# Optimization experiments

Measured on AMD Instinct MI355X. Metric: run time of the kernel, lower is better.

Reference implementation:

```python
import jax, jax.numpy as jnp
from jax import lax
import numpy as np

POINT_PAIRS = 10000
SIGMA = 0.03
ALPHA = 1.0
MIN_DEPTH = -0.001
MAX_DEPTH = 80.0


def _get_edges(images):
    # images: [n,3,H,W]; Sobel on channel 0, VALID conv then zero-pad by 1 (as in torch code)
    x = images[:, :1]
    kx = jnp.array([[-1., 0., 1.], [-2., 0., 2.], [-1., 0., 1.]], jnp.float32).reshape(1, 1, 3, 3)
    ky = jnp.array([[1., 2., 1.], [0., 0., 0.], [-1., -2., -1.]], jnp.float32).reshape(1, 1, 3, 3)
    gx = lax.conv_general_dilated(x, kx, (1, 1), 'VALID')
    gy = lax.conv_general_dilated(x, ky, (1, 1), 'VALID')
    edges = jnp.sqrt(gx * gx + gy * gy)
    thetas = jnp.arctan2(gy, gx)
    pad = ((0, 0), (0, 0), (1, 1), (1, 1))
    return jnp.pad(edges, pad), jnp.pad(thetas, pad)


def _sample_and_loss(key, inp, tgt, edge, theta, smask):
    # inp/tgt/edge/theta: [H,W] float; smask: [H,W] bool
    H, W = inp.shape
    k1, k2, k3 = jax.random.split(key, 3)
    # edge-guided anchor sampling: uniform over {edge >= 0.1*max} & strict_mask, with replacement
    emask = (edge >= 0.1 * edge.max()) & smask
    p = emask.reshape(-1).astype(jnp.float32)
    p = p / jnp.maximum(p.sum(), 1.0)
    flat_idx = jax.random.choice(k1, H * W, (POINT_PAIRS,), replace=True, p=p)
    sh = flat_idx // W
    sw = flat_idx % W
    th = theta.reshape(-1)[flat_idx]
    # signed step distances along / perpendicular to the edge direction
    dist = jax.random.randint(k2, (4, POINT_PAIRS), 2, 31).astype(jnp.float32)
    sign = jnp.array([-1., -1., 1., 1.], jnp.float32).reshape(4, 1)
    dist = dist * sign
    # random_direct: p<0.5 -> along gradient; else rotate theta by pi/2 (swapped cos/sin)
    pdir = jax.random.uniform(k3) < 0.5
    th2 = ((th + jnp.pi / 2) + jnp.pi) % (2 * jnp.pi) - jnp.pi
    col1 = sw[None, :] + jnp.round(dist * jnp.cos(th)[None, :]).astype(jnp.int32)
    row1 = sh[None, :] + jnp.round(dist * jnp.sin(th)[None, :]).astype(jnp.int32)
    col2 = sw[None, :] + jnp.round(dist * jnp.sin(th2)[None, :]).astype(jnp.int32)
    row2 = sh[None, :] + jnp.round(dist * jnp.cos(th2)[None, :]).astype(jnp.int32)
    col = jnp.where(pdir, col1, col2)  # [4,N]
    row = jnp.where(pdir, row1, row2)
    inb = (col >= 0) & (col <= W - 1) & (row >= 0) & (row <= H - 1)
    valid = jnp.all(inb, axis=0)  # [N]; torch drops these columns, we mask instead
    colc = jnp.clip(col, 0, W - 1)
    rowc = jnp.clip(row, 0, H - 1)
    # pairs (a,b),(b,c),(c,d) -> A = [a,b,c], B = [b,c,d]
    rA = jnp.concatenate([rowc[0], rowc[1], rowc[2]])
    cA = jnp.concatenate([colc[0], colc[1], colc[2]])
    rB = jnp.concatenate([rowc[1], rowc[2], rowc[3]])
    cB = jnp.concatenate([colc[1], colc[2], colc[3]])
    vm = jnp.concatenate([valid, valid, valid]).astype(jnp.float32)  # [3N]
    iA = inp[rA, cA]
    iB = inp[rB, cB]
    tA = tgt[rA, cA]
    tB = tgt[rB, cB]
    # ranking loss
    ratio = (tA + 1e-6) / (tB + 1e-6)
    absdiff = jnp.abs(tA - tB)
    maxdiff = jnp.max(jnp.where(vm > 0, absdiff, 0.0))
    tw = jnp.exp(absdiff / (maxdiff + 1e-6))
    eq = (ratio < 1.0 + SIGMA) & (ratio > 1.0 / (1.0 + SIGMA))
    labels = jnp.where(ratio >= 1.0 + SIGMA, 1.0,
                       jnp.where(ratio <= 1.0 / (1.0 + SIGMA), -1.0, 0.0))
    equal_loss = (iA - iB) ** 2 / tw * eq.astype(jnp.float32)
    unequal_loss = jnp.log1p(jnp.exp((iB - iA) * labels)) * (1.0 - eq.astype(jnp.float32))
    cnt = jnp.maximum(vm.sum(), 1.0)
    loss = ALPHA * jnp.sum(equal_loss * vm) / cnt + jnp.sum(unequal_loss * vm) / cnt
    return loss, vm.sum()


def setup_inputs() -> dict:
    key = jax.random.key(0)
    k1, k2, k3, k4 = jax.random.split(key, 4)
    n, H, W = 8, 1024, 1024
    inputs = jax.random.normal(k1, (n, 1, H, W), jnp.float32)
    targets = jax.random.uniform(k2, (n, 1, H, W), jnp.float32)
    images = jax.random.uniform(k3, (n, 3, H, W), jnp.float32)
    depth_gt = jax.random.uniform(k4, (n, 1, H, W), jnp.float32)
    return {"inputs": inputs, "targets": targets, "images": images, "depth_gt": depth_gt}


def reference(inputs, targets, images, depth_gt):
    n = inputs.shape[0]
    strict = (depth_gt > MIN_DEPTH) & (depth_gt < MAX_DEPTH) & ~(targets == 80.0)
    edges, thetas = _get_edges(images)
    keys = jax.random.split(jax.random.key(42), n)
    losses, counts = jax.vmap(_sample_and_loss)(
        keys, inputs[:, 0], targets[:, 0], edges[:, 0], thetas[:, 0], strict[:, 0])
    return losses.sum() / n, counts.sum() / n
```

## Files before the change

kernel.cpp:

```cpp
#include <hip/hip_runtime.h>
#include <math.h>
#include <stdint.h>

#define NIMG 8
#define HH 1024
#define WW 1024
#define NPIX (HH*WW)
#define PAIRS 10000
#define STRIP 8
#define NSTRIPS 128
#define S1BLOCKS 40
#define WSLOTS (S1BLOCKS*4)
#define FBLK 4
#define QPAIRS (PAIRS/FBLK)

#define OFF_EDGE 0
#define OFF_MD   1024
#define OFF_RES  4096
#define OFF_CTR  4112

__device__ __forceinline__ uint64_t mix64(uint64_t x){
    x += 0x9E3779B97F4A7C15ull;
    x = (x ^ (x >> 30)) * 0xBF58476D1CE4E5B9ull;
    x = (x ^ (x >> 27)) * 0x94D049BB133111EBull;
    return x ^ (x >> 31);
}

__device__ __forceinline__ float block_reduce_max(float v, float* sm){
    for (int off = 32; off; off >>= 1)
        v = fmaxf(v, __shfl_down(v, off));
    int wv = threadIdx.x >> 6, lane = threadIdx.x & 63;
    if (lane == 0) sm[wv] = v;
    __syncthreads();
    if (threadIdx.x == 0)
        sm[0] = fmaxf(fmaxf(sm[0], sm[1]), fmaxf(sm[2], sm[3]));
    __syncthreads();
    float r = sm[0];
    __syncthreads();
    return r;
}

__device__ __forceinline__ float block_reduce_sum(float v, float* sm){
    for (int off = 32; off; off >>= 1)
        v += __shfl_down(v, off);
    int wv = threadIdx.x >> 6, lane = threadIdx.x & 63;
    if (lane == 0) sm[wv] = v;
    __syncthreads();
    if (threadIdx.x == 0)
        sm[0] = sm[0] + sm[1] + sm[2] + sm[3];
    __syncthreads();
    float r = sm[0];
    __syncthreads();
    return r;
}

__device__ __forceinline__ void sobel_at(const float* __restrict__ x, int r, int c,
                                         float& gx, float& gy){
    const float* p0 = x + (size_t)(r-1)*WW + c;
    const float* p1 = x + (size_t)r*WW + c;
    const float* p2 = x + (size_t)(r+1)*WW + c;
    float a = p0[-1], b = p0[0], cc = p0[1];
    float d = p1[-1],             e = p1[1];
    float f = p2[-1], g = p2[0], h = p2[1];
    gx = (cc - a) + 2.0f*(e - d) + (h - f);
    gy = (a + 2.0f*b + cc) - (f + 2.0f*g + h);
}

__device__ __forceinline__ void load16(const float* __restrict__ p, float* d){
    const float4* q = (const float4*)p;
    float4 v0 = q[0], v1 = q[1], v2 = q[2], v3 = q[3];
    d[0]=v0.x; d[1]=v0.y; d[2]=v0.z; d[3]=v0.w;
    d[4]=v1.x; d[5]=v1.y; d[6]=v1.z; d[7]=v1.w;
    d[8]=v2.x; d[9]=v2.y; d[10]=v2.z; d[11]=v2.w;
    d[12]=v3.x; d[13]=v3.y; d[14]=v3.z; d[15]=v3.w;
}

__global__ __launch_bounds__(256) void edgemax_kernel(const float* __restrict__ images,
                                                      float* __restrict__ ws){
    if (blockIdx.x == 0 && threadIdx.x < 17)
        ws[OFF_RES + threadIdx.x] = 0.0f;

    int img  = blockIdx.x & 7;
    int xb   = blockIdx.x >> 3;
    const float* x = images + (size_t)img * 3 * NPIX;
    int wv   = threadIdx.x >> 6;
    int lane = threadIdx.x & 63;
    int strip = xb * 4 + wv;
    int r0 = 1 + strip * STRIP;
    int r1 = min(r0 + STRIP - 1, HH - 2);
    int c0 = lane * 16;

    float a[16], b[16], n[16];
    load16(x + (size_t)(r0-1)*WW + c0, a);
    load16(x + (size_t)r0*WW + c0, b);

    float m = 0.0f;
    for (int r = r0; r <= r1; ++r){
        load16(x + (size_t)(r+1)*WW + c0, n);
        float sx[16], dy[16];
        #pragma unroll
        for (int i = 0; i < 16; ++i){
            sx[i] = a[i] + 2.0f*b[i] + n[i];
            dy[i] = a[i] - n[i];
        }
        float sxl = __shfl_up(sx[15], 1);
        float sxr = __shfl_down(sx[0], 1);
        float dyl = __shfl_up(dy[15], 1);
        float dyr = __shfl_down(dy[0], 1);
        #pragma unroll
        for (int j = 0; j < 16; ++j){
            float sl = (j == 0)  ? sxl : sx[j-1];
            float sr = (j == 15) ? sxr : sx[j+1];
            float dl = (j == 0)  ? dyl : dy[j-1];
            float dr = (j == 15) ? dyr : dy[j+1];
            float gx = sr - sl;
            float gy = dl + 2.0f*dy[j] + dr;
            float e2 = gx*gx + gy*gy;
            int c = c0 + j;
            if (c >= 1 && c <= WW-2) m = fmaxf(m, e2);
        }
        #pragma unroll
        for (int i = 0; i < 16; ++i){ a[i] = b[i]; b[i] = n[i]; }
    }
    for (int off = 32; off; off >>= 1)
        m = fmaxf(m, __shfl_down(m, off));
    if (lane == 0)
        ws[OFF_EDGE + img * NSTRIPS + strip] = m;
}

__global__ __launch_bounds__(256) void sample_kernel(
                               const float* __restrict__ inputs,
                               const float* __restrict__ targets,
                               const float* __restrict__ images,
                               const float* __restrict__ depth_gt,
                               float* __restrict__ ws,
                               float4* __restrict__ recsA,
                               float4* __restrict__ recsB){
    __shared__ float sred[4];
    int img = blockIdx.x & 7;
    int jb  = blockIdx.x >> 3;
    int tid = threadIdx.x;
    int j   = jb * 256 + tid;
    const float* x   = images   + (size_t)img * 3 * NPIX;
    const float* inp = inputs   + (size_t)img * NPIX;
    const float* tgt = targets  + (size_t)img * NPIX;
    const float* dgt = depth_gt + (size_t)img * NPIX;

    float ev = 0.0f;
    if (tid < NSTRIPS) ev = ws[OFF_EDGE + img * NSTRIPS + tid];
    float thr2 = 0.01f * block_reduce_max(ev, sred);

    float mdiff = 0.0f;
    float4 recA = make_float4(0.f, 0.f, 0.f, 0.f);
    float4 recB = make_float4(0.f, 0.f, 0.f, 0.f);

    if (j < PAIRS){
        uint64_t base = ((uint64_t)(img * PAIRS + j)) << 10;
        bool pdir = (mix64(((uint64_t)(NIMG * PAIRS + img)) << 10) & 1ull) != 0ull;

        int sh = -1, sw = -1;
        float gxs = 0.f, gys = 0.f, e2s = 1.f;
        for (int att = 0; att < 900; ++att){
            uint64_t u = mix64(base + (uint64_t)att);
            uint32_t pix = (uint32_t)(u >> 44);
            int r = (int)(pix >> 10);
            int c = (int)(pix & (WW - 1));
            if (r == 0 || r >= HH-1 || c == 0 || c >= WW-1) continue;
            float gx, gy;
            sobel_at(x, r, c, gx, gy);
            float e2 = gx*gx + gy*gy;
            if (!(e2 >= thr2)) continue;
            float dg = dgt[r*WW + c];
            float tg = tgt[r*WW + c];
            if (!(dg > -0.001f && dg < 80.0f && tg != 80.0f)) continue;
            sh = r; sw = c; gxs = gx; gys = gy; e2s = e2;
            break;
        }

        if (sh >= 0){
            float inv = rsqrtf(e2s);
            float cmul = gxs * inv;
            float rmul = gys * inv;
            if (!pdir) cmul = -cmul;

            uint64_t u0 = mix64(base + 1000ull);
            uint64_t u1 = mix64(base + 1001ull);
            float dist[4];
            dist[0] = -(float)(2u + (uint32_t)(u0 & 0xFFFFFFFFull) % 29u);
            dist[1] = -(float)(2u + (uint32_t)(u0 >> 32) % 29u);
            dist[2] =  (float)(2u + (uint32_t)(u1 & 0xFFFFFFFFull) % 29u);
            dist[3] =  (float)(2u + (uint32_t)(u1 >> 32) % 29u);

            int rowc[4], colc[4];
            bool valid = true;
            #pragma unroll
            for (int k = 0; k < 4; ++k){
                int cc2 = sw + (int)rintf(dist[k] * cmul);
                int rr2 = sh + (int)rintf(dist[k] * rmul);
                if (cc2 < 0 || cc2 > WW-1 || rr2 < 0 || rr2 > HH-1) valid = false;
                colc[k] = min(max(cc2, 0), WW-1);
                rowc[k] = min(max(rr2, 0), HH-1);
            }

            if (valid){
                float t4[4], i4[4];
                #pragma unroll
                for (int k = 0; k < 4; ++k){
                    int p = rowc[k]*WW + colc[k];
                    t4[k] = tgt[p];
                    i4[k] = inp[p];
                }
                float d2a[3], ada[3];
                float un = 0.0f;
                #pragma unroll
                for (int k = 0; k < 3; ++k){
                    float tA = t4[k], tB = t4[k+1];
                    float ratio = (tA + 1e-6f) / (tB + 1e-6f);
                    float adk = fabsf(tA - tB);
                    mdiff = fmaxf(mdiff, adk);
                    bool eq = (ratio < 1.03f) && (ratio > 0.9708737864077669f);
                    if (eq){
                        float d = i4[k] - i4[k+1];
                        d2a[k] = d*d; ada[k] = adk;
                    } else {
                        d2a[k] = 0.f; ada[k] = 0.f;
                        float lab = (ratio >= 1.03f) ? 1.0f : -1.0f;
                        un += log1pf(expf((i4[k+1] - i4[k]) * lab));
                    }
                }
                recA = make_float4(d2a[0], d2a[1], d2a[2], un);
                recB = make_float4(ada[0], ada[1], ada[2], 3.0f);
            }
        }
        recsA[img * PAIRS + j] = recA;
        recsB[img * PAIRS + j] = recB;
    }

    for (int off = 32; off; off >>= 1)
        mdiff = fmaxf(mdiff, __shfl_down(mdiff, off));
    if ((tid & 63) == 0)
        ws[OFF_MD + img * WSLOTS + jb*4 + (tid >> 6)] = mdiff;
}

__global__ __launch_bounds__(256) void finish_kernel(
                               float* __restrict__ ws,
                               const float4* __restrict__ recsA,
                               const float4* __restrict__ recsB,
                               float* __restrict__ out){
    __shared__ float sred[4];
    __shared__ unsigned lastflag;
    int img = blockIdx.x & 7;
    int q   = blockIdx.x >> 3;
    int tid = threadIdx.x;

    float mv = 0.0f;
    if (tid < WSLOTS) mv = ws[OFF_MD + img * WSLOTS + tid];
    float md = block_reduce_max(mv, sred);
    float inv = 1.0f / (md + 1e-6f);

    float loss = 0.0f, cnt = 0.0f;
    int base = img * PAIRS + q * QPAIRS;
    for (int r = tid; r < QPAIRS; r += 256){
        float4 A = recsA[base + r];
        float4 B = recsB[base + r];
        loss += A.w
              + A.x * expf(-B.x * inv)
              + A.y * expf(-B.y * inv)
              + A.z * expf(-B.z * inv);
        cnt  += B.w;
    }
    loss = block_reduce_sum(loss, sred);
    cnt  = block_reduce_sum(cnt, sred);

    if (tid == 0){
        atomicAdd(&ws[OFF_RES + img*2 + 0], loss);
        atomicAdd(&ws[OFF_RES + img*2 + 1], cnt);
        __threadfence();
        unsigned old = atomicAdd((unsigned int*)&ws[OFF_CTR], 1u);
        lastflag = (old == (unsigned)(NIMG*FBLK - 1)) ? 1u : 0u;
    }
    __syncthreads();

    if (lastflag){
        __threadfence();
        float val = 0.0f, cv = 0.0f;
        if (tid < NIMG){
            float li = atomicAdd(&ws[OFF_RES + tid*2 + 0], 0.0f);
            float ci = atomicAdd(&ws[OFF_RES + tid*2 + 1], 0.0f);
            val = li / fmaxf(ci, 1.0f);
            cv  = ci;
        }
        for (int off = 4; off; off >>= 1){
            val += __shfl_down(val, off);
            cv  += __shfl_down(cv,  off);
        }
        if (tid == 0){
            out[0] = val / (float)NIMG;
            out[1] = cv  / (float)NIMG;
        }
    }
}

extern "C" void kernel_launch(void* const* d_in, const int* in_sizes, int n_in,
                              void* d_out, int out_size, void* d_ws, size_t ws_size,
                              hipStream_t stream) {
    const float* inputs  = (const float*)d_in[0];
    const float* targets = (const float*)d_in[1];
    const float* images  = (const float*)d_in[2];
    const float* depth   = (const float*)d_in[3];
    float* out = (float*)d_out;

    float* ws     = (float*)d_ws;
    float4* recsA = (float4*)((char*)d_ws + 65536);
    float4* recsB = recsA + (size_t)NIMG * PAIRS;

    hipLaunchKernelGGL(edgemax_kernel, dim3(NSTRIPS/4 * NIMG), dim3(256), 0, stream,
                       images, ws);
    hipLaunchKernelGGL(sample_kernel, dim3(S1BLOCKS * NIMG), dim3(256), 0, stream,
                       inputs, targets, images, depth, ws, recsA, recsB);
    hipLaunchKernelGGL(finish_kernel, dim3(NIMG * FBLK), dim3(256), 0, stream,
                       ws, recsA, recsB, out);
}
```

Before: 38.25 us.

## Fuse finish reduction into sample kernel via last-block-per-image atomics

Merges the separate finish kernel into the sample kernel. Each block publishes its max depth difference with an atomicMax and bumps a per-image counter, and the last block for each image does that image's loss reduction. A second counter picks the final block, which writes the outputs. This removes one kernel launch and its gap, but the per-image tail reduction now runs on one block per image (8 blocks) instead of 32. It also depends on atomic ordering through s_waitcnt instead of a full threadfence.

```diff
diff --git a/kernel.cpp b/kernel.cpp
--- a/kernel.cpp
+++ b/kernel.cpp
@@ -10,14 +10,14 @@
 #define STRIP 8
 #define NSTRIPS 128
 #define S1BLOCKS 40
-#define WSLOTS (S1BLOCKS*4)
-#define FBLK 4
-#define QPAIRS (PAIRS/FBLK)
 
 #define OFF_EDGE 0
-#define OFF_MD   1024
-#define OFF_RES  4096
-#define OFF_CTR  4112
+#define OFF_MDI  4096
+#define OFF_DONE 4104
+#define OFF_GL   4112
+#define OFF_GC   4113
+#define OFF_IMGD 4114
+#define ZERO_N   24
 
 __device__ __forceinline__ uint64_t mix64(uint64_t x){
     x += 0x9E3779B97F4A7C15ull;
@@ -77,8 +77,8 @@
 
 __global__ __launch_bounds__(256) void edgemax_kernel(const float* __restrict__ images,
                                                       float* __restrict__ ws){
-    if (blockIdx.x == 0 && threadIdx.x < 17)
-        ws[OFF_RES + threadIdx.x] = 0.0f;
+    if (blockIdx.x == 0 && threadIdx.x < ZERO_N)
+        ws[OFF_MDI + threadIdx.x] = 0.0f;
 
     int img  = blockIdx.x & 7;
     int xb   = blockIdx.x >> 3;
@@ -128,15 +128,17 @@
         ws[OFF_EDGE + img * NSTRIPS + strip] = m;
 }
 
-__global__ __launch_bounds__(256) void sample_kernel(
+__global__ __launch_bounds__(256) void sample_finish_kernel(
                                const float* __restrict__ inputs,
                                const float* __restrict__ targets,
                                const float* __restrict__ images,
                                const float* __restrict__ depth_gt,
                                float* __restrict__ ws,
                                float4* __restrict__ recsA,
-                               float4* __restrict__ recsB){
+                               float4* __restrict__ recsB,
+                               float* __restrict__ out){
     __shared__ float sred[4];
+    __shared__ unsigned flag1;
     int img = blockIdx.x & 7;
     int jb  = blockIdx.x >> 3;
     int tid = threadIdx.x;
@@ -236,67 +238,45 @@
         recsB[img * PAIRS + j] = recB;
     }
 
-    for (int off = 32; off; off >>= 1)
-        mdiff = fmaxf(mdiff, __shfl_down(mdiff, off));
-    if ((tid & 63) == 0)
-        ws[OFF_MD + img * WSLOTS + jb*4 + (tid >> 6)] = mdiff;
-}
-
-__global__ __launch_bounds__(256) void finish_kernel(
-                               float* __restrict__ ws,
-                               const float4* __restrict__ recsA,
-                               const float4* __restrict__ recsB,
-                               float* __restrict__ out){
-    __shared__ float sred[4];
-    __shared__ unsigned lastflag;
-    int img = blockIdx.x & 7;
-    int q   = blockIdx.x >> 3;
-    int tid = threadIdx.x;
-
-    float mv = 0.0f;
-    if (tid < WSLOTS) mv = ws[OFF_MD + img * WSLOTS + tid];
-    float md = block_reduce_max(mv, sred);
-    float inv = 1.0f / (md + 1e-6f);
-
-    float loss = 0.0f, cnt = 0.0f;
-    int base = img * PAIRS + q * QPAIRS;
-    for (int r = tid; r < QPAIRS; r += 256){
-        float4 A = recsA[base + r];
-        float4 B = recsB[base + r];
-        loss += A.w
-              + A.x * expf(-B.x * inv)
-              + A.y * expf(-B.y * inv)
-              + A.z * expf(-B.z * inv);
-        cnt  += B.w;
+    float mdb = block_reduce_max(mdiff, sred);
+    if (tid == 0){
+        if (mdb > 0.0f)
+            atomicMax((unsigned int*)&ws[OFF_MDI + img], __float_as_uint(mdb));
+        asm volatile("s_waitcnt vmcnt(0)" ::: "memory");
+        unsigned old = atomicAdd((unsigned int*)&ws[OFF_DONE + img], 1u);
+        flag1 = (old == (unsigned)(S1BLOCKS - 1)) ? 1u : 0u;
     }
-    loss = block_reduce_sum(loss, sred);
-    cnt  = block_reduce_sum(cnt, sred);
-
-    if (tid == 0){
-        atomicAdd(&ws[OFF_RES + img*2 + 0], loss);
-        atomicAdd(&ws[OFF_RES + img*2 + 1], cnt);
-        __threadfence();
-        unsigned old = atomicAdd((unsigned int*)&ws[OFF_CTR], 1u);
-        lastflag = (old == (unsigned)(NIMG*FBLK - 1)) ? 1u : 0u;
-    }
-    __syncthreads();
-
-    if (lastflag){
-        __threadfence();
-        float val = 0.0f, cv = 0.0f;
-        if (tid < NIMG){
-            float li = atomicAdd(&ws[OFF_RES + tid*2 + 0], 0.0f);
-            float ci = atomicAdd(&ws[OFF_RES + tid*2 + 1], 0.0f);
-            val = li / fmaxf(ci, 1.0f);
-            cv  = ci;
-        }
-        for (int off = 4; off; off >>= 1){
-            val += __shfl_down(val, off);
-            cv  += __shfl_down(cv,  off);
-        }
+    __syncthreads();
+
+    if (flag1){
+        float md = __uint_as_float(atomicAdd((unsigned int*)&ws[OFF_MDI + img], 0u));
+        float inv = 1.0f / (md + 1e-6f);
+
+        float loss = 0.0f, cnt = 0.0f;
+        for (int r = tid; r < PAIRS; r += 256){
+            float4 A = recsA[img * PAIRS + r];
+            float4 B = recsB[img * PAIRS + r];
+            loss += A.w
+                  + A.x * expf(-B.x * inv)
+                  + A.y * expf(-B.y * inv)
+                  + A.z * expf(-B.z * inv);
+            cnt  += B.w;
+        }
+        loss = block_reduce_sum(loss, sred);
+        cnt  = block_reduce_sum(cnt, sred);
+
         if (tid == 0){
-            out[0] = val / (float)NIMG;
-            out[1] = cv  / (float)NIMG;
+            float Li = loss / fmaxf(cnt, 1.0f);
+            atomicAdd(&ws[OFF_GL], Li);
+            atomicAdd(&ws[OFF_GC], cnt);
+            asm volatile("s_waitcnt vmcnt(0)" ::: "memory");
+            unsigned o2 = atomicAdd((unsigned int*)&ws[OFF_IMGD], 1u);
+            if (o2 == (unsigned)(NIMG - 1)){
+                float gl = atomicAdd(&ws[OFF_GL], 0.0f);
+                float gc = atomicAdd(&ws[OFF_GC], 0.0f);
+                out[0] = gl / (float)NIMG;
+                out[1] = gc / (float)NIMG;
+            }
         }
     }
 }
@@ -316,8 +296,6 @@
 
     hipLaunchKernelGGL(edgemax_kernel, dim3(NSTRIPS/4 * NIMG), dim3(256), 0, stream,
                        images, ws);
-    hipLaunchKernelGGL(sample_kernel, dim3(S1BLOCKS * NIMG), dim3(256), 0, stream,
-                       inputs, targets, images, depth, ws, recsA, recsB);
-    hipLaunchKernelGGL(finish_kernel, dim3(NIMG * FBLK), dim3(256), 0, stream,
-                       ws, recsA, recsB, out);
-}
+    hipLaunchKernelGGL(sample_finish_kernel, dim3(S1BLOCKS * NIMG), dim3(256), 0, stream,
+                       inputs, targets, images, depth, ws, recsA, recsB, out);
+}
```

After: 50.58 us. 1.32x slower.

## Software-pipeline rejection-sampling loads and pad per-image atomic accumulators

Applied to the files above, without the earlier changes.

The rejection-sampling loop now issues the Sobel neighbourhood, depth and target loads for the next candidate pixel before evaluating the current one. Border pixels are clamped so those loads stay in bounds, and the acceptance test checks the clamped coordinates against the originals. This is meant to hide global-memory latency in the serial sampling loop, at the cost of extra registers and always-issued loads, including one wasted prefetch at loop exit. Per-image loss and count accumulators are also spread to 32-float strides, with the counter moved and zeroed, to cut atomic contention on shared cache lines.

```diff
diff --git a/kernel.cpp b/kernel.cpp
--- a/kernel.cpp
+++ b/kernel.cpp
@@ -17,7 +17,7 @@
 #define OFF_EDGE 0
 #define OFF_MD   1024
 #define OFF_RES  4096
-#define OFF_CTR  4112
+#define OFF_CTR  4352
 
 __device__ __forceinline__ uint64_t mix64(uint64_t x){
     x += 0x9E3779B97F4A7C15ull;
@@ -52,18 +52,6 @@
     float r = sm[0];
     __syncthreads();
     return r;
-}
-
-__device__ __forceinline__ void sobel_at(const float* __restrict__ x, int r, int c,
-                                         float& gx, float& gy){
-    const float* p0 = x + (size_t)(r-1)*WW + c;
-    const float* p1 = x + (size_t)r*WW + c;
-    const float* p2 = x + (size_t)(r+1)*WW + c;
-    float a = p0[-1], b = p0[0], cc = p0[1];
-    float d = p1[-1],             e = p1[1];
-    float f = p2[-1], g = p2[0], h = p2[1];
-    gx = (cc - a) + 2.0f*(e - d) + (h - f);
-    gy = (a + 2.0f*b + cc) - (f + 2.0f*g + h);
 }
 
 __device__ __forceinline__ void load16(const float* __restrict__ p, float* d){
@@ -77,8 +65,10 @@
 
 __global__ __launch_bounds__(256) void edgemax_kernel(const float* __restrict__ images,
                                                       float* __restrict__ ws){
-    if (blockIdx.x == 0 && threadIdx.x < 17)
+    if (blockIdx.x == 0){
         ws[OFF_RES + threadIdx.x] = 0.0f;
+        if (threadIdx.x == 0) ws[OFF_CTR] = 0.0f;
+    }
 
     int img  = blockIdx.x & 7;
     int xb   = blockIdx.x >> 3;
@@ -126,6 +116,31 @@
         m = fmaxf(m, __shfl_down(m, off));
     if (lane == 0)
         ws[OFF_EDGE + img * NSTRIPS + strip] = m;
+}
+
+struct AttLd {
+    int r, c, rl, cl;
+    float a, b, cc, d, e, f, g, h, dg, tg;
+};
+
+__device__ __forceinline__ AttLd att_issue(uint64_t u,
+        const float* __restrict__ x, const float* __restrict__ tgt,
+        const float* __restrict__ dgt){
+    AttLd s;
+    uint32_t pix = (uint32_t)(u >> 44);
+    s.r  = (int)(pix >> 10);
+    s.c  = (int)(pix & (WW - 1));
+    s.rl = min(max(s.r, 1), HH-2);
+    s.cl = min(max(s.c, 1), WW-2);
+    const float* p0 = x + (size_t)(s.rl-1)*WW + s.cl;
+    const float* p1 = x + (size_t)s.rl*WW + s.cl;
+    const float* p2 = x + (size_t)(s.rl+1)*WW + s.cl;
+    s.a = p0[-1]; s.b = p0[0]; s.cc = p0[1];
+    s.d = p1[-1];               s.e = p1[1];
+    s.f = p2[-1]; s.g = p2[0];  s.h = p2[1];
+    s.dg = dgt[s.rl*WW + s.cl];
+    s.tg = tgt[s.rl*WW + s.cl];
+    return s;
 }
 
 __global__ __launch_bounds__(256) void sample_kernel(
@@ -160,21 +175,20 @@
 
         int sh = -1, sw = -1;
         float gxs = 0.f, gys = 0.f, e2s = 1.f;
+
+        AttLd cur = att_issue(mix64(base + 0ull), x, tgt, dgt);
         for (int att = 0; att < 900; ++att){
-            uint64_t u = mix64(base + (uint64_t)att);
-            uint32_t pix = (uint32_t)(u >> 44);
-            int r = (int)(pix >> 10);
-            int c = (int)(pix & (WW - 1));
-            if (r == 0 || r >= HH-1 || c == 0 || c >= WW-1) continue;
-            float gx, gy;
-            sobel_at(x, r, c, gx, gy);
+            AttLd nxt = att_issue(mix64(base + (uint64_t)(att + 1)), x, tgt, dgt);
+            float gx = (cur.cc - cur.a) + 2.0f*(cur.e - cur.d) + (cur.h - cur.f);
+            float gy = (cur.a + 2.0f*cur.b + cur.cc) - (cur.f + 2.0f*cur.g + cur.h);
             float e2 = gx*gx + gy*gy;
-            if (!(e2 >= thr2)) continue;
-            float dg = dgt[r*WW + c];
-            float tg = tgt[r*WW + c];
-            if (!(dg > -0.001f && dg < 80.0f && tg != 80.0f)) continue;
-            sh = r; sw = c; gxs = gx; gys = gy; e2s = e2;
-            break;
+            bool pass = (cur.r == cur.rl) && (cur.c == cur.cl) && (e2 >= thr2) &&
+                        (cur.dg > -0.001f && cur.dg < 80.0f) && (cur.tg != 80.0f);
+            if (pass){
+                sh = cur.rl; sw = cur.cl; gxs = gx; gys = gy; e2s = e2;
+                break;
+            }
+            cur = nxt;
         }
 
         if (sh >= 0){
@@ -273,8 +287,8 @@
     cnt  = block_reduce_sum(cnt, sred);
 
     if (tid == 0){
-        atomicAdd(&ws[OFF_RES + img*2 + 0], loss);
-        atomicAdd(&ws[OFF_RES + img*2 + 1], cnt);
+        atomicAdd(&ws[OFF_RES + img*32 + 0], loss);
+        atomicAdd(&ws[OFF_RES + img*32 + 1], cnt);
         __threadfence();
         unsigned old = atomicAdd((unsigned int*)&ws[OFF_CTR], 1u);
         lastflag = (old == (unsigned)(NIMG*FBLK - 1)) ? 1u : 0u;
@@ -285,8 +299,8 @@
         __threadfence();
         float val = 0.0f, cv = 0.0f;
         if (tid < NIMG){
-            float li = atomicAdd(&ws[OFF_RES + tid*2 + 0], 0.0f);
-            float ci = atomicAdd(&ws[OFF_RES + tid*2 + 1], 0.0f);
+            float li = atomicAdd(&ws[OFF_RES + tid*32 + 0], 0.0f);
+            float ci = atomicAdd(&ws[OFF_RES + tid*32 + 1], 0.0f);
             val = li / fmaxf(ci, 1.0f);
             cv  = ci;
         }
```

After: 38.20 us. Within noise of the previous version (-0.1%).
